# Performance work log

Hardware: AMD Instinct MI355X
Metric: run time of the kernel (lower is better)

The kernel has to match this reference:

```python
import jax, jax.numpy as jnp
import numpy as np

N = 4096      # num nodes
F = 64        # input feature dim
H = 8         # head_num
D = 8         # att_embedding_size


def setup_inputs() -> dict:
    key = jax.random.key(0)
    k1, k2, k3, k4, k5, k6 = jax.random.split(key, 6)
    X = jax.random.normal(k1, (N, F), dtype=jnp.float32)
    # sparse-ish binary adjacency with self loops (avg degree ~ 41)
    A = (jax.random.uniform(k2, (N, N)) < 0.01).astype(jnp.float32)
    A = jnp.maximum(A, jnp.eye(N, dtype=jnp.float32))
    # glorot-uniform-ish parameter init
    lim_w = np.sqrt(6.0 / (F + H * D)).astype(np.float32)
    W = jax.random.uniform(k3, (F, H * D), minval=-lim_w, maxval=lim_w, dtype=jnp.float32)
    lim_a = np.sqrt(6.0 / (1 + H * D)).astype(np.float32)
    att_self = jax.random.uniform(k4, (H, D), minval=-lim_a, maxval=lim_a, dtype=jnp.float32)
    att_neigh = jax.random.uniform(k5, (H, D), minval=-lim_a, maxval=lim_a, dtype=jnp.float32)
    bias = jnp.zeros((H, D), dtype=jnp.float32)
    return {"X": X, "A": A, "W": W, "att_self": att_self, "att_neigh": att_neigh, "bias": bias}


def reference(X, A, W, att_self, att_neigh, bias):
    # features: [N, H, D]
    feats = (X @ W).reshape(-1, H, D)
    # additive attention logits per node/head: [N, H]
    a_self = jnp.einsum('nhd,hd->nh', feats, att_self)
    a_neigh = jnp.einsum('nhd,hd->nh', feats, att_neigh)
    # scores[h, i, j] = a_self[i, h] + a_neigh[j, h]  -> [H, N, N]
    scores = a_self.T[:, :, None] + a_neigh.T[:, None, :]
    scores = jax.nn.leaky_relu(scores, negative_slope=0.2)
    # adjacency mask: -1e10 where no edge
    scores = scores + (-1e10 * (1.0 - A))[None, :, :]
    attn = jax.nn.softmax(scores, axis=-1)           # [H, N, N]
    # aggregate: [H, N, N] x [N, H, D] -> [N, H, D]
    out = jnp.einsum('hij,jhd->ihd', attn, feats)
    out = out + bias[None, :, :]                     # use_bias
    out = out.reshape(-1, H * D)                     # reduction='concat'
    return jax.nn.relu(out)                          # activation=relu
```

## Files before the change

kernel.cpp:

```cpp
#include <hip/hip_runtime.h>
#include <hip/hip_bf16.h>

#define NNODES 4096
#define NF 64
#define NH 8
#define ND 8
#define HD 64
#define EMAX 128

__device__ __forceinline__ float ldv(const void* p, int i, bool f32) {
    return f32 ? ((const float*)p)[i]
               : __bfloat162float(((const __hip_bfloat16*)p)[i]);
}

__device__ __forceinline__ void ld8(const void* base, int idx, bool f32, float* o) {
    if (f32) {
        const float4* p = (const float4*)((const float*)base + idx);
        float4 a = p[0], b = p[1];
        o[0]=a.x; o[1]=a.y; o[2]=a.z; o[3]=a.w;
        o[4]=b.x; o[5]=b.y; o[6]=b.z; o[7]=b.w;
    } else {
        uint4 u = *(const uint4*)((const unsigned short*)base + idx);
        unsigned int ws[4] = {u.x, u.y, u.z, u.w};
        #pragma unroll
        for (int q = 0; q < 4; ++q) {
            o[2*q]   = __uint_as_float(ws[q] << 16);
            o[2*q+1] = __uint_as_float(ws[q] & 0xffff0000u);
        }
    }
}

__device__ __forceinline__ bool a_is_f32(const void* A) {
    return *(const unsigned int*)A == 0x3F800000u;
}

__global__ __launch_bounds__(256) void gat_fused(
    const void* __restrict__ X,
    const void* __restrict__ W,
    const void* __restrict__ att_self,
    const void* __restrict__ att_neigh,
    const void* __restrict__ A,
    float* __restrict__ feats,
    float* __restrict__ a_self,
    float* __restrict__ a_neigh,
    unsigned short* __restrict__ elist,
    int* __restrict__ ecnt)
{
    const bool f32 = a_is_f32(A);
    const int t = threadIdx.x;
    __shared__ float Wl[NF][HD];
    __shared__ float Xl[4][NF];
    __shared__ int wtot[4];

    if (blockIdx.x < NNODES / 4) {
        {
            float wv[16];
            ld8(W, t * 16,     f32, wv);
            ld8(W, t * 16 + 8, f32, wv + 8);
            const int row = t >> 2, col0 = (t & 3) * 16;
            #pragma unroll
            for (int k = 0; k < 16; ++k) Wl[row][col0 + k] = wv[k];
        }
        if (t < 32) {
            const int row = t >> 3, col = (t & 7) * 8;
            float xv[8];
            ld8(X, (blockIdx.x * 4 + row) * NF + col, f32, xv);
            #pragma unroll
            for (int k = 0; k < 8; ++k) Xl[row][col + k] = xv[k];
        }
        __syncthreads();

        const int r = t >> 6, c = t & 63;
        float acc = 0.f;
        #pragma unroll
        for (int k = 0; k < NF; ++k)
            acc = fmaf(Xl[r][k], Wl[k][c], acc);

        const int n = blockIdx.x * 4 + r;
        feats[n * HD + c] = acc;

        const int d = c & 7, h = c >> 3;
        float vs = acc * ldv(att_self, c, f32);
        float vn = acc * ldv(att_neigh, c, f32);
        #pragma unroll
        for (int off = 1; off < 8; off <<= 1) {
            vs += __shfl_xor(vs, off, 64);
            vn += __shfl_xor(vn, off, 64);
        }
        if (d == 0) {
            a_self[n * NH + h]  = vs;
            a_neigh[n * NH + h] = vn;
        }
    } else {
        const int i = blockIdx.x - NNODES / 4;
        const int wave = t >> 6, lane = t & 63;

        unsigned int bits = 0;
        if (f32) {
            const uint4* ap = (const uint4*)((const float*)A + (size_t)i * NNODES + t * 16);
            #pragma unroll
            for (int q = 0; q < 4; ++q) {
                uint4 p = ap[q];
                if (p.x) bits |= 1u << (4 * q + 0);
                if (p.y) bits |= 1u << (4 * q + 1);
                if (p.z) bits |= 1u << (4 * q + 2);
                if (p.w) bits |= 1u << (4 * q + 3);
            }
        } else {
            const uint4* ap = (const uint4*)((const unsigned short*)A + (size_t)i * NNODES + t * 16);
            uint4 p0 = ap[0], p1 = ap[1];
            unsigned int w0[4] = {p0.x, p0.y, p0.z, p0.w};
            unsigned int w1[4] = {p1.x, p1.y, p1.z, p1.w};
            #pragma unroll
            for (int q = 0; q < 4; ++q) {
                if (w0[q] & 0x0000ffffu) bits |= 1u << (2 * q);
                if (w0[q] & 0xffff0000u) bits |= 1u << (2 * q + 1);
                if (w1[q] & 0x0000ffffu) bits |= 1u << (8 + 2 * q);
                if (w1[q] & 0xffff0000u) bits |= 1u << (8 + 2 * q + 1);
            }
        }

        int cnt = __popc(bits);
        int incl = cnt;
        #pragma unroll
        for (int off = 1; off < 64; off <<= 1) {
            int nn = __shfl_up(incl, off, 64);
            if (lane >= off) incl += nn;
        }
        if (lane == 63) wtot[wave] = incl;
        __syncthreads();
        int base = 0;
        #pragma unroll
        for (int w = 0; w < 4; ++w) if (w < wave) base += wtot[w];

        int off0 = base + (incl - cnt);
        unsigned int mb = bits;
        while (mb) {
            int b = __ffs(mb) - 1; mb &= mb - 1;
            if (off0 < EMAX) elist[i * EMAX + off0] = (unsigned short)(t * 16 + b);
            ++off0;
        }
        if (t == 0) {
            int tot = wtot[0] + wtot[1] + wtot[2] + wtot[3];
            ecnt[i] = (tot < EMAX) ? tot : EMAX;
        }
    }
}

__global__ __launch_bounds__(256) void gat_gather(
    const unsigned short* __restrict__ elist,
    const int* __restrict__ ecnt,
    const float* __restrict__ feats,
    const float* __restrict__ a_self_g,
    const float* __restrict__ a_neigh,
    const void* __restrict__ bias,
    const void* __restrict__ A,
    float* __restrict__ out)
{
    const bool f32 = a_is_f32(A);
    const int i = blockIdx.x;
    const int t = threadIdx.x;
    const int wave = t >> 6, lane = t & 63;
    const int c = lane, h = c >> 3, d = c & 7;

    __shared__ float red[4][HD];
    __shared__ float dsh[4][NH];

    const float ash = a_self_g[i * NH + h];
    const int nE = ecnt[i];
    const unsigned short* el = elist + i * EMAX;

    const int cntw = (nE > wave) ? ((nE - 1 - wave) >> 2) + 1 : 0;
    float acc = 0.f, den = 0.f;

    for (int m0 = 0; m0 < cntw; m0 += 8) {
        int j[8];
        #pragma unroll
        for (int k = 0; k < 8; ++k) {
            int e = wave + 4 * (m0 + k);
            e = (e < nE) ? e : (wave + 4 * m0);
            j[k] = el[e];
        }
        float an[8], fv[8];
        #pragma unroll
        for (int k = 0; k < 8; ++k) an[k] = a_neigh[j[k] * NH + h];
        #pragma unroll
        for (int k = 0; k < 8; ++k) fv[k] = feats[j[k] * HD + c];
        #pragma unroll
        for (int k = 0; k < 8; ++k)
            if (m0 + k >= cntw) an[k] = -1e30f;
        #pragma unroll
        for (int k = 0; k < 8; ++k) {
            float s = ash + an[k];
            s = (s >= 0.f) ? s : 0.2f * s;
            float wt = __expf(s);
            acc = fmaf(wt, fv[k], acc);
            den += wt;
        }
    }

    red[wave][c] = acc;
    if (d == 0) dsh[wave][h] = den;
    __syncthreads();

    if (t < HD) {
        float tot = red[0][t] + red[1][t] + red[2][t] + red[3][t];
        float dd = dsh[0][t >> 3] + dsh[1][t >> 3] + dsh[2][t >> 3] + dsh[3][t >> 3];
        float v = tot / dd + ldv(bias, t, f32);
        out[(size_t)i * HD + t] = fmaxf(v, 0.f);
    }
}

extern "C" void kernel_launch(void* const* d_in, const int* in_sizes, int n_in,
                              void* d_out, int out_size, void* d_ws, size_t ws_size,
                              hipStream_t stream) {
    const void* X         = d_in[0];
    const void* A         = d_in[1];
    const void* W         = d_in[2];
    const void* att_self  = d_in[3];
    const void* att_neigh = d_in[4];
    const void* bias      = d_in[5];
    float* out = (float*)d_out;

    float* feats   = (float*)d_ws;
    float* a_self  = feats  + NNODES * HD;
    float* a_neigh = a_self + NNODES * NH;
    int*   ecnt    = (int*)(a_neigh + NNODES * NH);
    unsigned short* elist = (unsigned short*)(ecnt + NNODES);

    gat_fused<<<NNODES / 4 + NNODES, 256, 0, stream>>>(
        X, W, att_self, att_neigh, A, feats, a_self, a_neigh, elist, ecnt);
    gat_gather<<<NNODES, 256, 0, stream>>>(
        elist, ecnt, feats, a_self, a_neigh, bias, A, out);
}
```

Baseline: 26.88 us.

## Use per-wave edge segments and fully unrolled 16-edge gather batches

Each wave in the adjacency scan now writes its neighbours into its own fixed 32-slot segment with a byte count, removing the cross-wave shared-memory prefix and block barrier. The gather kernel reads a wave's segment with vector loads and processes up to 16 edges per batch fully unrolled, with a second batch only when needed. This aims to raise memory-level parallelism and cut sync overhead. In exchange, it risks dropping edges when a 1024-column quarter holds more than 32 neighbours, and it wastes loads on padded slots.

```diff
diff --git a/kernel.cpp b/kernel.cpp
--- a/kernel.cpp
+++ b/kernel.cpp
@@ -7,6 +7,7 @@
 #define ND 8
 #define HD 64
 #define EMAX 128
+#define SCAP 32
 
 __device__ __forceinline__ float ldv(const void* p, int i, bool f32) {
     return f32 ? ((const float*)p)[i]
@@ -44,13 +45,12 @@
     float* __restrict__ a_self,
     float* __restrict__ a_neigh,
     unsigned short* __restrict__ elist,
-    int* __restrict__ ecnt)
+    unsigned int* __restrict__ ecnt4)
 {
     const bool f32 = a_is_f32(A);
     const int t = threadIdx.x;
     __shared__ float Wl[NF][HD];
     __shared__ float Xl[4][NF];
-    __shared__ int wtot[4];
 
     if (blockIdx.x < NNODES / 4) {
         {
@@ -94,10 +94,11 @@
     } else {
         const int i = blockIdx.x - NNODES / 4;
         const int wave = t >> 6, lane = t & 63;
+        const int col0 = wave * 1024 + lane * 16;
 
         unsigned int bits = 0;
         if (f32) {
-            const uint4* ap = (const uint4*)((const float*)A + (size_t)i * NNODES + t * 16);
+            const uint4* ap = (const uint4*)((const float*)A + (size_t)i * NNODES + col0);
             #pragma unroll
             for (int q = 0; q < 4; ++q) {
                 uint4 p = ap[q];
@@ -107,7 +108,7 @@
                 if (p.w) bits |= 1u << (4 * q + 3);
             }
         } else {
-            const uint4* ap = (const uint4*)((const unsigned short*)A + (size_t)i * NNODES + t * 16);
+            const uint4* ap = (const uint4*)((const unsigned short*)A + (size_t)i * NNODES + col0);
             uint4 p0 = ap[0], p1 = ap[1];
             unsigned int w0[4] = {p0.x, p0.y, p0.z, p0.w};
             unsigned int w1[4] = {p1.x, p1.y, p1.z, p1.w};
@@ -127,29 +128,24 @@
             int nn = __shfl_up(incl, off, 64);
             if (lane >= off) incl += nn;
         }
-        if (lane == 63) wtot[wave] = incl;
-        __syncthreads();
-        int base = 0;
-        #pragma unroll
-        for (int w = 0; w < 4; ++w) if (w < wave) base += wtot[w];
-
-        int off0 = base + (incl - cnt);
+        int pos = incl - cnt;
+        unsigned short* seg = elist + i * EMAX + wave * SCAP;
         unsigned int mb = bits;
         while (mb) {
             int b = __ffs(mb) - 1; mb &= mb - 1;
-            if (off0 < EMAX) elist[i * EMAX + off0] = (unsigned short)(t * 16 + b);
-            ++off0;
-        }
-        if (t == 0) {
-            int tot = wtot[0] + wtot[1] + wtot[2] + wtot[3];
-            ecnt[i] = (tot < EMAX) ? tot : EMAX;
+            if (pos < SCAP) seg[pos] = (unsigned short)(col0 + b);
+            ++pos;
+        }
+        if (lane == 63) {
+            int tot = (incl < SCAP) ? incl : SCAP;
+            ((unsigned char*)ecnt4)[i * 4 + wave] = (unsigned char)tot;
         }
     }
 }
 
 __global__ __launch_bounds__(256) void gat_gather(
     const unsigned short* __restrict__ elist,
-    const int* __restrict__ ecnt,
+    const unsigned int* __restrict__ ecnt4,
     const float* __restrict__ feats,
     const float* __restrict__ a_self_g,
     const float* __restrict__ a_neigh,
@@ -166,38 +162,63 @@
     __shared__ float red[4][HD];
     __shared__ float dsh[4][NH];
 
+    const unsigned short* seg = elist + i * EMAX + wave * SCAP;
+    uint4 id0 = ((const uint4*)seg)[0];
+    uint4 id1 = ((const uint4*)seg)[1];
+    const unsigned int cnts = ecnt4[i];
     const float ash = a_self_g[i * NH + h];
-    const int nE = ecnt[i];
-    const unsigned short* el = elist + i * EMAX;
-
-    const int cntw = (nE > wave) ? ((nE - 1 - wave) >> 2) + 1 : 0;
+    const int cw = (cnts >> (wave * 8)) & 0xff;
+
     float acc = 0.f, den = 0.f;
 
-    for (int m0 = 0; m0 < cntw; m0 += 8) {
-        int j[8];
-        #pragma unroll
-        for (int k = 0; k < 8; ++k) {
-            int e = wave + 4 * (m0 + k);
-            e = (e < nE) ? e : (wave + 4 * m0);
-            j[k] = el[e];
-        }
-        float an[8], fv[8];
-        #pragma unroll
-        for (int k = 0; k < 8; ++k) an[k] = a_neigh[j[k] * NH + h];
-        #pragma unroll
-        for (int k = 0; k < 8; ++k) fv[k] = feats[j[k] * HD + c];
-        #pragma unroll
-        for (int k = 0; k < 8; ++k)
-            if (m0 + k >= cntw) an[k] = -1e30f;
-        #pragma unroll
-        for (int k = 0; k < 8; ++k) {
-            float s = ash + an[k];
+    {
+        unsigned int q[8] = {id0.x, id0.y, id0.z, id0.w, id1.x, id1.y, id1.z, id1.w};
+        int j[16];
+        #pragma unroll
+        for (int k = 0; k < 16; ++k) {
+            int id = (q[k >> 1] >> ((k & 1) * 16)) & 0xffff;
+            j[k] = (k < cw) ? id : i;
+        }
+        float an[16], fv[16];
+        #pragma unroll
+        for (int k = 0; k < 16; ++k) an[k] = a_neigh[j[k] * NH + h];
+        #pragma unroll
+        for (int k = 0; k < 16; ++k) fv[k] = feats[j[k] * HD + c];
+        #pragma unroll
+        for (int k = 0; k < 16; ++k) {
+            float aa = (k < cw) ? an[k] : -1e30f;
+            float s = ash + aa;
             s = (s >= 0.f) ? s : 0.2f * s;
             float wt = __expf(s);
             acc = fmaf(wt, fv[k], acc);
             den += wt;
         }
     }
+    if (cw > 16) {
+        uint4 id2 = ((const uint4*)seg)[2];
+        uint4 id3 = ((const uint4*)seg)[3];
+        unsigned int q[8] = {id2.x, id2.y, id2.z, id2.w, id3.x, id3.y, id3.z, id3.w};
+        int j[16];
+        #pragma unroll
+        for (int k = 0; k < 16; ++k) {
+            int id = (q[k >> 1] >> ((k & 1) * 16)) & 0xffff;
+            j[k] = (16 + k < cw) ? id : i;
+        }
+        float an[16], fv[16];
+        #pragma unroll
+        for (int k = 0; k < 16; ++k) an[k] = a_neigh[j[k] * NH + h];
+        #pragma unroll
+        for (int k = 0; k < 16; ++k) fv[k] = feats[j[k] * HD + c];
+        #pragma unroll
+        for (int k = 0; k < 16; ++k) {
+            float aa = (16 + k < cw) ? an[k] : -1e30f;
+            float s = ash + aa;
+            s = (s >= 0.f) ? s : 0.2f * s;
+            float wt = __expf(s);
+            acc = fmaf(wt, fv[k], acc);
+            den += wt;
+        }
+    }
 
     red[wave][c] = acc;
     if (d == 0) dsh[wave][h] = den;
@@ -205,7 +226,8 @@
 
     if (t < HD) {
         float tot = red[0][t] + red[1][t] + red[2][t] + red[3][t];
-        float dd = dsh[0][t >> 3] + dsh[1][t >> 3] + dsh[2][t >> 3] + dsh[3][t >> 3];
+        int hh = t >> 3;
+        float dd = dsh[0][hh] + dsh[1][hh] + dsh[2][hh] + dsh[3][hh];
         float v = tot / dd + ldv(bias, t, f32);
         out[(size_t)i * HD + t] = fmaxf(v, 0.f);
     }
@@ -225,11 +247,11 @@
     float* feats   = (float*)d_ws;
     float* a_self  = feats  + NNODES * HD;
     float* a_neigh = a_self + NNODES * NH;
-    int*   ecnt    = (int*)(a_neigh + NNODES * NH);
-    unsigned short* elist = (unsigned short*)(ecnt + NNODES);
+    unsigned int* ecnt4 = (unsigned int*)(a_neigh + NNODES * NH);
+    unsigned short* elist = (unsigned short*)(ecnt4 + NNODES);
 
     gat_fused<<<NNODES / 4 + NNODES, 256, 0, stream>>>(
-        X, W, att_self, att_neigh, A, feats, a_self, a_neigh, elist, ecnt);
+        X, W, att_self, att_neigh, A, feats, a_self, a_neigh, elist, ecnt4);
     gat_gather<<<NNODES, 256, 0, stream>>>(
-        elist, ecnt, feats, a_self, a_neigh, bias, A, out);
-}
+        elist, ecnt4, feats, a_self, a_neigh, bias, A, out);
+}
```

Measured after the change: 27.84 us. +3.6%, slower.
